# Kernel optimization log

Hardware: AMD Instinct MI355X
Metric: run time of the kernel (lower is better)

The kernel has to match this reference:

```python
import jax, jax.numpy as jnp
import numpy as np


def _pool2(x):
    # 2x2 max pool, stride 2 (matches F.max_pool2d(x, 2))
    b, c, h, w = x.shape
    return x.reshape(b, c, h // 2, 2, w // 2, 2).max(axis=(3, 5))


def setup_inputs() -> dict:
    key = jax.random.key(0)
    ks = jax.random.split(key, 6)
    B, C, H, W = 16, 512, 64, 64
    x = jax.random.normal(ks[0], (B, C, H, W), dtype=jnp.float32)
    scale = 0.02
    theta_w = jax.random.normal(ks[1], (C // 8, C), dtype=jnp.float32) * scale
    phi_w = jax.random.normal(ks[2], (C // 8, C), dtype=jnp.float32) * scale
    g_w = jax.random.normal(ks[3], (C // 2, C), dtype=jnp.float32) * scale
    o_w = jax.random.normal(ks[4], (C, C // 2), dtype=jnp.float32) * scale
    # original inits gamma=0; use a nonzero value so output depends on attention path
    gamma = jax.random.normal(ks[5], (), dtype=jnp.float32) * 0.5
    return {"x": x, "theta_w": theta_w, "phi_w": phi_w, "g_w": g_w, "o_w": o_w, "gamma": gamma}


def reference(x, theta_w, phi_w, g_w, o_w, gamma):
    B, C, H, W = x.shape
    HW = H * W
    # 1x1 convs == channel GEMMs
    theta = jnp.einsum('bchw,kc->bkhw', x, theta_w).reshape(B, C // 8, HW).transpose(0, 2, 1)  # [B, HW, C/8]
    phi = _pool2(jnp.einsum('bchw,kc->bkhw', x, phi_w)).reshape(B, C // 8, HW // 4)            # [B, C/8, HW/4]
    beta = jax.nn.softmax(jnp.einsum('bnk,bkm->bnm', theta, phi), axis=-1)                     # [B, HW, HW/4]
    g = _pool2(jnp.einsum('bchw,kc->bkhw', x, g_w)).reshape(B, C // 2, HW // 4)                # [B, C/2, HW/4]
    # g.bmm(beta^T): contract over pooled positions m -> [B, C/2, HW]
    o_in = jnp.einsum('bcm,bnm->bcn', g, beta).reshape(B, C // 2, H, W)
    o = jnp.einsum('bchw,kc->bkhw', o_in, o_w)                                                 # [B, C, H, W]
    return gamma * o + x
```

## Files before the change

### kernel.cpp

```cpp
#include <hip/hip_runtime.h>

#define B_   16
#define C_   512
#define HW_  4096
#define M_   1024
#define TPAD 136

typedef __attribute__((ext_vector_type(8))) short bf16x8;
typedef __attribute__((ext_vector_type(4))) float f32x4;

static __device__ __forceinline__ unsigned short f2bf(float f) {
    union { float f; unsigned u; } v; v.f = f;
    unsigned r = v.u + 0x7fffu + ((v.u >> 16) & 1u);
    return (unsigned short)(r >> 16);
}
static __device__ __forceinline__ float bf2f(unsigned short h) {
    union { unsigned u; float f; } v; v.u = ((unsigned)h) << 16;
    return v.f;
}
static __device__ __forceinline__ void gload_lds16(const void* g, void* l) {
    __builtin_amdgcn_global_load_lds(
        (const __attribute__((address_space(1))) unsigned int*)g,
        (__attribute__((address_space(3))) unsigned int*)l, 16, 0, 0);
}
static __device__ __forceinline__ unsigned cvt_pk(float lo, float hi) {
    unsigned r;
    asm("v_cvt_pk_bf16_f32 %0, %1, %2" : "=v"(r) : "v"(lo), "v"(hi));
    return r;
}

__global__ __launch_bounds__(256) void k_weights(
    const float* __restrict__ thw, const float* __restrict__ phw,
    const float* __restrict__ gw,  const float* __restrict__ ow,
    unsigned short* __restrict__ Wb, unsigned short* __restrict__ oWb) {
    int i = blockIdx.x * 256 + threadIdx.x;
    if (i < 32768)        Wb[i] = f2bf(thw[i]);
    else if (i < 65536)   Wb[i] = f2bf(phw[i - 32768]);
    else if (i < 196608)  Wb[i] = f2bf(gw[i - 65536]);
    else if (i < 327680)  oWb[i - 196608] = f2bf(ow[i - 196608]);
}

__global__ __launch_bounds__(512, 2) void k_proj(
    const float* __restrict__ x, const unsigned short* __restrict__ Wb,
    unsigned short* __restrict__ theta_n, unsigned short* __restrict__ phi_p,
    unsigned short* __restrict__ g_p) {
    __shared__ float xlds[2][64 * 128];
    __shared__ unsigned short smem[128 * TPAD];

    int b = blockIdx.y, bx = blockIdx.x;
    int hw0 = bx * 128;
    int tid = threadIdx.x, w = tid >> 6, lane = tid & 63;
    int l15 = lane & 15, q = lane >> 4;
    int rg = w >> 1, cg = w & 1;

    const float* xb = x + (size_t)b * C_ * HW_ + hw0;

#define STAGEX(ks_, buf_)                                                      \
    _Pragma("unroll")                                                          \
    for (int i = 0; i < 4; i++) {                                              \
        int u = i * 512 + tid;                                                 \
        int c = u >> 5, chunk = u & 31;                                        \
        int swz = ((c >> 3) & 1) << 4;                                         \
        gload_lds16(xb + (size_t)((ks_) * 64 + c) * HW_ + ((chunk * 4) ^ swz), \
                    &xlds[buf_][(i * 512 + w * 64) * 4]);                      \
    }

    STAGEX(0, 0);
    __syncthreads();

    f32x4 acc[6][4] = {};
    for (int ks = 0; ks < 8; ks++) {
        int cur = ks & 1;
        bf16x8 af[2][6];
#pragma unroll
        for (int kk = 0; kk < 2; kk++)
#pragma unroll
            for (int mi = 0; mi < 6; mi++) {
                int row = rg * 96 + mi * 16 + l15;
                af[kk][mi] = *(const bf16x8*)(Wb + (size_t)row * 512 + ks * 64 + kk * 32 + q * 8);
            }
        if (ks < 7) { STAGEX(ks + 1, cur ^ 1); }
#pragma unroll
        for (int kk = 0; kk < 2; kk++) {
#pragma unroll
            for (int ni = 0; ni < 4; ni++) {
                int colsw = (cg * 64 + ni * 16 + l15) ^ ((q & 1) << 4);
                const float* base = &xlds[cur][(kk * 32 + q * 8) * 128 + colsw];
                float f0 = base[0],   f1 = base[128], f2 = base[256], f3 = base[384];
                float f4 = base[512], f5 = base[640], f6 = base[768], f7 = base[896];
                bf16x8 bfr;
                unsigned* bw = (unsigned*)&bfr;
                bw[0] = cvt_pk(f0, f1); bw[1] = cvt_pk(f2, f3);
                bw[2] = cvt_pk(f4, f5); bw[3] = cvt_pk(f6, f7);
#pragma unroll
                for (int mi = 0; mi < 6; mi++)
                    acc[mi][ni] = __builtin_amdgcn_mfma_f32_16x16x32_bf16(
                        af[kk][mi], bfr, acc[mi][ni], 0, 0, 0);
            }
        }
        __syncthreads();
    }
#undef STAGEX

    for (int t = 0; t < 3; t++) {
        __syncthreads();
#pragma unroll
        for (int mi = 0; mi < 6; mi++) {
            int grow = rg * 96 + mi * 16;
            if ((grow >> 7) == t) {
#pragma unroll
                for (int ni = 0; ni < 4; ni++) {
                    int col = cg * 64 + ni * 16 + l15;
                    int row = (grow & 127) + q * 4;
                    ushort4 u;
                    u.x = f2bf(acc[mi][ni][0]); u.y = f2bf(acc[mi][ni][1]);
                    u.z = f2bf(acc[mi][ni][2]); u.w = f2bf(acc[mi][ni][3]);
                    *reinterpret_cast<ushort4*>(&smem[col * TPAD + row]) = u;
                }
            }
        }
        __syncthreads();

        if (t == 0) {
            int hw_l = tid >> 2, kh = (tid & 3) * 16;
            const unsigned short* srcp = &smem[hw_l * TPAD + kh];
            unsigned short* dstp = theta_n + ((size_t)b * HW_ + hw0 + hw_l) * 64 + kh;
            *reinterpret_cast<uint4*>(dstp)     = *reinterpret_cast<const uint4*>(srcp);
            *reinterpret_cast<uint4*>(dstp + 8) = *reinterpret_cast<const uint4*>(srcp + 8);
            int pc = tid & 63, mg = tid >> 6;
#pragma unroll
            for (int j = 0; j < 4; j++) {
                int m_l = mg * 4 + j, w_ = m_l * 2;
                float v0 = bf2f(smem[(w_)      * TPAD + 64 + pc]);
                float v1 = bf2f(smem[(w_ + 1)  * TPAD + 64 + pc]);
                float v2 = bf2f(smem[(64 + w_) * TPAD + 64 + pc]);
                float v3 = bf2f(smem[(65 + w_) * TPAD + 64 + pc]);
                float v = fmaxf(fmaxf(v0, v1), fmaxf(v2, v3));
                phi_p[((size_t)b * M_ + bx * 32 + m_l) * 64 + pc] = f2bf(v);
            }
        } else {
            int lr = tid & 127, mq = tid >> 7;
            int gc = (t - 1) * 128 + lr;
            unsigned short* dst = g_p + ((size_t)b * 256 + gc) * M_ + bx * 32 + mq * 8;
            unsigned short tmp[8];
#pragma unroll
            for (int i = 0; i < 8; i++) {
                int w_ = (mq * 8 + i) * 2;
                float v0 = bf2f(smem[(w_)      * TPAD + lr]);
                float v1 = bf2f(smem[(w_ + 1)  * TPAD + lr]);
                float v2 = bf2f(smem[(64 + w_) * TPAD + lr]);
                float v3 = bf2f(smem[(65 + w_) * TPAD + lr]);
                tmp[i] = f2bf(fmaxf(fmaxf(v0, v1), fmaxf(v2, v3)));
            }
            *reinterpret_cast<ushort4*>(dst)     = *reinterpret_cast<const ushort4*>(&tmp[0]);
            *reinterpret_cast<ushort4*>(dst + 4) = *reinterpret_cast<const ushort4*>(&tmp[4]);
        }
    }
}

__global__ __launch_bounds__(256, 2) void k_attn(
    const unsigned short* __restrict__ theta_n, const unsigned short* __restrict__ phi_p,
    const unsigned short* __restrict__ g_p, unsigned short* __restrict__ o_in) {
    __shared__ unsigned short phi_s[64 * 64];
    __shared__ unsigned short g_s[256 * 64];
    __shared__ unsigned short p_lds[4][32][68];

    int b = blockIdx.y, n0 = blockIdx.x * 128;
    int tid = threadIdx.x, w = tid >> 6, lane = tid & 63;
    int l15 = lane & 15, q = lane >> 4;
    int nw = n0 + w * 32;

    const unsigned short* th = theta_n + ((size_t)b * HW_ + nw + l15) * 64 + q * 8;
    bf16x8 a[2][2];
    a[0][0] = *(const bf16x8*)(th);            a[0][1] = *(const bf16x8*)(th + 32);
    a[1][0] = *(const bf16x8*)(th + 16 * 64);  a[1][1] = *(const bf16x8*)(th + 16 * 64 + 32);

    const unsigned short* phib = phi_p + (size_t)b * M_ * 64;
    const unsigned short* gb   = g_p   + (size_t)b * 256 * M_;

    bf16x8 ones;
    {
        short v = (l15 == 0) ? (short)0x3F80 : (short)0;
#pragma unroll
        for (int i = 0; i < 8; i++) ones[i] = v;
    }

    int sw = l15 & 7;

    f32x4 acc[2][17] = {};
    for (int mc = 0; mc < 16; mc++) {
        int m0 = mc * 64;
        __syncthreads();
#pragma unroll
        for (int i = 0; i < 2; i++) {
            int u = i * 256 + tid;
            int row = u >> 3, ch = (lane & 7) ^ (row & 7);
            gload_lds16(phib + (size_t)(m0 + row) * 64 + ch * 8,
                        &phi_s[(i * 256 + w * 64) * 8]);
        }
#pragma unroll
        for (int i = 0; i < 8; i++) {
            int u = i * 256 + tid;
            int row = u >> 3, ch = (lane & 7) ^ (row & 7);
            gload_lds16(gb + (size_t)row * M_ + m0 + ch * 8,
                        &g_s[(i * 256 + w * 64) * 8]);
        }
        __syncthreads();

#pragma unroll
        for (int f = 0; f < 4; f++) {
            const unsigned short* pr = &phi_s[(f * 16 + l15) * 64];
            bf16x8 b0 = *(const bf16x8*)(pr + (q ^ sw) * 8);
            bf16x8 b1 = *(const bf16x8*)(pr + ((q + 4) ^ sw) * 8);
#pragma unroll
            for (int t = 0; t < 2; t++) {
                f32x4 s = {};
                s = __builtin_amdgcn_mfma_f32_16x16x32_bf16(a[t][0], b0, s, 0, 0, 0);
                s = __builtin_amdgcn_mfma_f32_16x16x32_bf16(a[t][1], b1, s, 0, 0, 0);
#pragma unroll
                for (int j = 0; j < 4; j++)
                    p_lds[w][t * 16 + q * 4 + j][f * 16 + l15] = f2bf(__expf(s[j]));
            }
        }
        bf16x8 p[2][2];
#pragma unroll
        for (int t = 0; t < 2; t++) {
            p[t][0] = *(const bf16x8*)&p_lds[w][t * 16 + l15][q * 8];
            p[t][1] = *(const bf16x8*)&p_lds[w][t * 16 + l15][32 + q * 8];
        }
#pragma unroll
        for (int cf = 0; cf < 16; cf++) {
            const unsigned short* gr = &g_s[(cf * 16 + l15) * 64];
            bf16x8 g0 = *(const bf16x8*)(gr + (q ^ sw) * 8);
            bf16x8 g1 = *(const bf16x8*)(gr + ((q + 4) ^ sw) * 8);
#pragma unroll
            for (int t = 0; t < 2; t++) {
                acc[t][cf] = __builtin_amdgcn_mfma_f32_16x16x32_bf16(p[t][0], g0, acc[t][cf], 0, 0, 0);
                acc[t][cf] = __builtin_amdgcn_mfma_f32_16x16x32_bf16(p[t][1], g1, acc[t][cf], 0, 0, 0);
            }
        }
#pragma unroll
        for (int t = 0; t < 2; t++) {
            acc[t][16] = __builtin_amdgcn_mfma_f32_16x16x32_bf16(p[t][0], ones, acc[t][16], 0, 0, 0);
            acc[t][16] = __builtin_amdgcn_mfma_f32_16x16x32_bf16(p[t][1], ones, acc[t][16], 0, 0, 0);
        }
    }

#pragma unroll
    for (int t = 0; t < 2; t++) {
        float dinv[4];
#pragma unroll
        for (int j = 0; j < 4; j++) {
            float d = __shfl(acc[t][16][j], (lane & 48), 64);
            dinv[j] = 1.0f / d;
        }
#pragma unroll
        for (int cf = 0; cf < 16; cf++)
#pragma unroll
            for (int j = 0; j < 4; j++)
                o_in[((size_t)b * HW_ + nw + t * 16 + q * 4 + j) * 256 + cf * 16 + l15] =
                    f2bf(acc[t][cf][j] * dinv[j]);
    }
}

__global__ __launch_bounds__(256, 4) void k_oproj(
    const unsigned short* __restrict__ o_in, const unsigned short* __restrict__ oWb,
    const float* __restrict__ x, const float* __restrict__ gamma_p,
    float* __restrict__ out) {
    __shared__ unsigned short smem[128 * TPAD];
    unsigned short* As = smem;
    unsigned short* Bs = smem + 8192;

    int b = blockIdx.z, mt = blockIdx.y, hw0 = blockIdx.x * 128;
    int tid = threadIdx.x, w = tid >> 6, lane = tid & 63;
    int l15 = lane & 15, q = lane >> 4;
    int wr = w >> 1, wc = w & 1;

    const unsigned short* Ab = oWb + (size_t)(mt * 128) * 256;
    const unsigned short* Bb = o_in + ((size_t)b * HW_ + hw0) * 256;
    int trow = tid >> 3, tch = tid & 7;

    f32x4 acc[4][4] = {};
    for (int ks = 0; ks < 4; ks++) {
        int k0 = ks * 64;
        if (ks) __syncthreads();
#pragma unroll
        for (int i = 0; i < 4; i++) {
            int row = i * 32 + trow;
            int ch = tch ^ (row & 7);
            gload_lds16(Ab + (size_t)row * 256 + k0 + ch * 8, &As[(i * 256 + w * 64) * 8]);
        }
#pragma unroll
        for (int i = 0; i < 4; i++) {
            int row = i * 32 + trow;
            int ch = tch ^ (row & 7);
            gload_lds16(Bb + (size_t)row * 256 + k0 + ch * 8, &Bs[(i * 256 + w * 64) * 8]);
        }
        __syncthreads();
#pragma unroll
        for (int kk = 0; kk < 2; kk++) {
            bf16x8 af[4], bfr[4];
#pragma unroll
            for (int mi = 0; mi < 4; mi++) {
                int row = wr * 64 + mi * 16 + l15;
                int ch = (kk * 4 + q) ^ (row & 7);
                af[mi] = *(const bf16x8*)&As[row * 64 + ch * 8];
            }
#pragma unroll
            for (int ni = 0; ni < 4; ni++) {
                int row = wc * 64 + ni * 16 + l15;
                int ch = (kk * 4 + q) ^ (row & 7);
                bfr[ni] = *(const bf16x8*)&Bs[row * 64 + ch * 8];
            }
#pragma unroll
            for (int mi = 0; mi < 4; mi++)
#pragma unroll
                for (int ni = 0; ni < 4; ni++)
                    acc[mi][ni] = __builtin_amdgcn_mfma_f32_16x16x32_bf16(
                        af[mi], bfr[ni], acc[mi][ni], 0, 0, 0);
        }
    }

    __syncthreads();
#pragma unroll
    for (int mi = 0; mi < 4; mi++)
#pragma unroll
        for (int ni = 0; ni < 4; ni++) {
            int col = wc * 64 + ni * 16 + l15;
            int rb = wr * 64 + mi * 16 + q * 4;
#pragma unroll
            for (int j = 0; j < 4; j++)
                smem[(rb + j) * TPAD + col] = f2bf(acc[mi][ni][j]);
        }
    __syncthreads();

    float gam = *gamma_p;
    int sub = tid >> 5, p32 = tid & 31;
#pragma unroll
    for (int p = 0; p < 16; p++) {
        int row = p * 8 + sub;
        ushort4 v = *reinterpret_cast<const ushort4*>(&smem[row * TPAD + p32 * 4]);
        size_t idx = ((size_t)b * C_ + mt * 128 + row) * HW_ + hw0 + p32 * 4;
        float4 xv = *reinterpret_cast<const float4*>(x + idx);
        float4 o;
        o.x = gam * bf2f(v.x) + xv.x;
        o.y = gam * bf2f(v.y) + xv.y;
        o.z = gam * bf2f(v.z) + xv.z;
        o.w = gam * bf2f(v.w) + xv.w;
        *reinterpret_cast<float4*>(out + idx) = o;
    }
}

extern "C" void kernel_launch(void* const* d_in, const int* in_sizes, int n_in,
                              void* d_out, int out_size, void* d_ws, size_t ws_size,
                              hipStream_t stream) {
    const float* x     = (const float*)d_in[0];
    const float* thw   = (const float*)d_in[1];
    const float* phw   = (const float*)d_in[2];
    const float* gw    = (const float*)d_in[3];
    const float* ow    = (const float*)d_in[4];
    const float* gamma = (const float*)d_in[5];
    float* out = (float*)d_out;

    char* ws = (char*)d_ws;
    unsigned short* Wb   = (unsigned short*)(ws + 0);
    unsigned short* oWb  = (unsigned short*)(ws + 393216);
    unsigned short* oin  = (unsigned short*)(ws + 655360);
    unsigned short* thn  = (unsigned short*)(ws + 34209792);
    unsigned short* phip = (unsigned short*)(ws + 42598400);
    unsigned short* gp   = (unsigned short*)(ws + 44695552);

    hipLaunchKernelGGL(k_weights, dim3(1280), dim3(256), 0, stream, thw, phw, gw, ow, Wb, oWb);
    hipLaunchKernelGGL(k_proj, dim3(32, 16), dim3(512), 0, stream, x, Wb, thn, phip, gp);
    hipLaunchKernelGGL(k_attn, dim3(32, 16), dim3(256), 0, stream, thn, phip, gp, oin);
    hipLaunchKernelGGL(k_oproj, dim3(32, 4, 16), dim3(256), 0, stream, oin, oWb, x, gamma, out);
}
```

Before: 192.2 us.

## Pre-transpose x to bf16 HW-major layout before projection GEMM

Adds a separate kernel that transposes x from [B,C,HW] fp32 into [B,HW,C] bf16, and rewrites the projection GEMM to stage this bf16 operand into LDS with 16-byte vector reads and an XOR swizzle. This replaces per-element fp32 LDS reads and bf16 packing in the inner loop. The cost is an extra kernel launch plus a full pass that reads 128MB of x and writes 64MB back to workspace. The GEMM then reads half as many bytes of x and has a simpler inner loop.

```diff
diff --git a/kernel.cpp b/kernel.cpp
--- a/kernel.cpp
+++ b/kernel.cpp
@@ -22,11 +22,6 @@
     __builtin_amdgcn_global_load_lds(
         (const __attribute__((address_space(1))) unsigned int*)g,
         (__attribute__((address_space(3))) unsigned int*)l, 16, 0, 0);
-}
-static __device__ __forceinline__ unsigned cvt_pk(float lo, float hi) {
-    unsigned r;
-    asm("v_cvt_pk_bf16_f32 %0, %1, %2" : "=v"(r) : "v"(lo), "v"(hi));
-    return r;
 }
 
 __global__ __launch_bounds__(256) void k_weights(
@@ -40,12 +35,39 @@
     else if (i < 327680)  oWb[i - 196608] = f2bf(ow[i - 196608]);
 }
 
+__global__ __launch_bounds__(256) void k_transpose_x(
+    const float* __restrict__ x, unsigned short* __restrict__ xT) {
+    __shared__ float tile[64][65];
+    int b = blockIdx.z, c0 = blockIdx.y * 64, hw0 = blockIdx.x * 64;
+    const float* xb = x + ((size_t)b * C_ + c0) * HW_ + hw0;
+    int t = threadIdx.x;
+    int r = t >> 4, c4 = (t & 15) * 4;
+#pragma unroll
+    for (int k = 0; k < 4; k++) {
+        int row = r + k * 16;
+        float4 v = *reinterpret_cast<const float4*>(xb + (size_t)row * HW_ + c4);
+        tile[row][c4 + 0] = v.x; tile[row][c4 + 1] = v.y;
+        tile[row][c4 + 2] = v.z; tile[row][c4 + 3] = v.w;
+    }
+    __syncthreads();
+    unsigned short* o = xT + ((size_t)b * HW_ + hw0) * C_ + c0;
+#pragma unroll
+    for (int k = 0; k < 4; k++) {
+        int hwr = r + k * 16;
+        ushort4 u;
+        u.x = f2bf(tile[c4 + 0][hwr]); u.y = f2bf(tile[c4 + 1][hwr]);
+        u.z = f2bf(tile[c4 + 2][hwr]); u.w = f2bf(tile[c4 + 3][hwr]);
+        *reinterpret_cast<ushort4*>(o + (size_t)hwr * C_ + c4) = u;
+    }
+}
+
 __global__ __launch_bounds__(512, 2) void k_proj(
-    const float* __restrict__ x, const unsigned short* __restrict__ Wb,
+    const unsigned short* __restrict__ xT, const unsigned short* __restrict__ Wb,
     unsigned short* __restrict__ theta_n, unsigned short* __restrict__ phi_p,
     unsigned short* __restrict__ g_p) {
-    __shared__ float xlds[2][64 * 128];
     __shared__ unsigned short smem[128 * TPAD];
+    unsigned short* Bs0 = smem;
+    unsigned short* Bs1 = smem + 8192;
 
     int b = blockIdx.y, bx = blockIdx.x;
     int hw0 = bx * 128;
@@ -53,24 +75,25 @@
     int l15 = lane & 15, q = lane >> 4;
     int rg = w >> 1, cg = w & 1;
 
-    const float* xb = x + (size_t)b * C_ * HW_ + hw0;
-
-#define STAGEX(ks_, buf_)                                                      \
+    const unsigned short* Bb = xT + ((size_t)b * HW_ + hw0) * C_;
+
+#define STAGEB(ks_, dst_)                                                      \
     _Pragma("unroll")                                                          \
-    for (int i = 0; i < 4; i++) {                                              \
+    for (int i = 0; i < 2; i++) {                                              \
         int u = i * 512 + tid;                                                 \
-        int c = u >> 5, chunk = u & 31;                                        \
-        int swz = ((c >> 3) & 1) << 4;                                         \
-        gload_lds16(xb + (size_t)((ks_) * 64 + c) * HW_ + ((chunk * 4) ^ swz), \
-                    &xlds[buf_][(i * 512 + w * 64) * 4]);                      \
-    }
-
-    STAGEX(0, 0);
-    __syncthreads();
+        int row = u >> 3, ch = (u & 7) ^ (row & 7);                            \
+        gload_lds16(Bb + (size_t)row * 512 + (ks_) * 64 + ch * 8,              \
+                    &(dst_)[(i * 512 + w * 64) * 8]);                          \
+    }
+
+    STAGEB(0, Bs0);
 
     f32x4 acc[6][4] = {};
+#pragma unroll
     for (int ks = 0; ks < 8; ks++) {
-        int cur = ks & 1;
+        unsigned short* cur = (ks & 1) ? Bs1 : Bs0;
+        unsigned short* nxt = (ks & 1) ? Bs0 : Bs1;
+        __syncthreads();
         bf16x8 af[2][6];
 #pragma unroll
         for (int kk = 0; kk < 2; kk++)
@@ -79,28 +102,25 @@
                 int row = rg * 96 + mi * 16 + l15;
                 af[kk][mi] = *(const bf16x8*)(Wb + (size_t)row * 512 + ks * 64 + kk * 32 + q * 8);
             }
-        if (ks < 7) { STAGEX(ks + 1, cur ^ 1); }
+        if (ks < 7) { STAGEB(ks + 1, nxt); }
 #pragma unroll
         for (int kk = 0; kk < 2; kk++) {
+            bf16x8 bfr[4];
 #pragma unroll
             for (int ni = 0; ni < 4; ni++) {
-                int colsw = (cg * 64 + ni * 16 + l15) ^ ((q & 1) << 4);
-                const float* base = &xlds[cur][(kk * 32 + q * 8) * 128 + colsw];
-                float f0 = base[0],   f1 = base[128], f2 = base[256], f3 = base[384];
-                float f4 = base[512], f5 = base[640], f6 = base[768], f7 = base[896];
-                bf16x8 bfr;
-                unsigned* bw = (unsigned*)&bfr;
-                bw[0] = cvt_pk(f0, f1); bw[1] = cvt_pk(f2, f3);
-                bw[2] = cvt_pk(f4, f5); bw[3] = cvt_pk(f6, f7);
-#pragma unroll
-                for (int mi = 0; mi < 6; mi++)
+                int row = cg * 64 + ni * 16 + l15;
+                int ch = (kk * 4 + q) ^ (row & 7);
+                bfr[ni] = *(const bf16x8*)&cur[row * 64 + ch * 8];
+            }
+#pragma unroll
+            for (int mi = 0; mi < 6; mi++)
+#pragma unroll
+                for (int ni = 0; ni < 4; ni++)
                     acc[mi][ni] = __builtin_amdgcn_mfma_f32_16x16x32_bf16(
-                        af[kk][mi], bfr, acc[mi][ni], 0, 0, 0);
-            }
-        }
-        __syncthreads();
-    }
-#undef STAGEX
+                        af[kk][mi], bfr[ni], acc[mi][ni], 0, 0, 0);
+        }
+    }
+#undef STAGEB
 
     for (int t = 0; t < 3; t++) {
         __syncthreads();
@@ -363,15 +383,17 @@
     float* out = (float*)d_out;
 
     char* ws = (char*)d_ws;
-    unsigned short* Wb   = (unsigned short*)(ws + 0);
-    unsigned short* oWb  = (unsigned short*)(ws + 393216);
-    unsigned short* oin  = (unsigned short*)(ws + 655360);
-    unsigned short* thn  = (unsigned short*)(ws + 34209792);
-    unsigned short* phip = (unsigned short*)(ws + 42598400);
-    unsigned short* gp   = (unsigned short*)(ws + 44695552);
+    unsigned short* xT   = (unsigned short*)(ws + 0);
+    unsigned short* Wb   = (unsigned short*)(ws + 67108864);
+    unsigned short* oWb  = (unsigned short*)(ws + 67502080);
+    unsigned short* oin  = (unsigned short*)(ws + 67764224);
+    unsigned short* thn  = (unsigned short*)(ws + 101318656);
+    unsigned short* phip = (unsigned short*)(ws + 109707264);
+    unsigned short* gp   = (unsigned short*)(ws + 111804416);
 
     hipLaunchKernelGGL(k_weights, dim3(1280), dim3(256), 0, stream, thw, phw, gw, ow, Wb, oWb);
-    hipLaunchKernelGGL(k_proj, dim3(32, 16), dim3(512), 0, stream, x, Wb, thn, phip, gp);
+    hipLaunchKernelGGL(k_transpose_x, dim3(64, 8, 16), dim3(256), 0, stream, x, xT);
+    hipLaunchKernelGGL(k_proj, dim3(32, 16), dim3(512), 0, stream, xT, Wb, thn, phip, gp);
     hipLaunchKernelGGL(k_attn, dim3(32, 16), dim3(256), 0, stream, thn, phip, gp, oin);
     hipLaunchKernelGGL(k_oproj, dim3(32, 4, 16), dim3(256), 0, stream, oin, oWb, x, gamma, out);
 }
```

Measured after the change: 220.5 us. +14.8%, slower.
